# Kernel optimization log

Measured on AMD Instinct MI355X. Metric: run time of the kernel, lower is better.

The kernel has to match this reference:

```python
import jax, jax.numpy as jnp
import numpy as np

B = 16      # number of point clouds
N = 4096    # points per cloud (max after densify)
D = 3       # xyz


def setup_inputs() -> dict:
    key = jax.random.key(0)
    k1, k2 = jax.random.split(key)
    pred = jax.random.normal(k1, (B * N, D), dtype=jnp.float32)
    target = jax.random.normal(k2, (B * N, D), dtype=jnp.float32)
    # sorted segment ids, equal-sized clouds (faithful to to_dense_batch usage)
    batch = jnp.repeat(jnp.arange(B, dtype=jnp.int64), N)
    return {"pred": pred, "target": target, "batch": batch}


def to_dense_batch(x, batch, num_batches, max_n):
    # PyG to_dense_batch: scatter flat points into [B, max_n, D], zero-padded.
    ones = jnp.ones_like(batch)
    counts = jax.ops.segment_sum(ones, batch, num_segments=num_batches)
    offsets = jnp.concatenate([jnp.zeros((1,), batch.dtype), jnp.cumsum(counts)[:-1]])
    pos = jnp.arange(batch.shape[0], dtype=batch.dtype) - offsets[batch]
    dense = jnp.zeros((num_batches, max_n, x.shape[-1]), x.dtype)
    return dense.at[batch, pos].set(x)


def chamfer_distance(x, y):
    # squared-euclidean pairwise distances via the GEMM identity
    x2 = jnp.sum(x * x, axis=-1)                      # [B, N]
    y2 = jnp.sum(y * y, axis=-1)                      # [B, M]
    xy = jnp.einsum('bnd,bmd->bnm', x, y)             # [B, N, M]
    d = x2[:, :, None] + y2[:, None, :] - 2.0 * xy    # [B, N, M]
    cham_x = jnp.mean(jnp.min(d, axis=2), axis=1)     # mean over N of min over M
    cham_y = jnp.mean(jnp.min(d, axis=1), axis=1)     # mean over M of min over N
    # point_reduction='mean', batch_reduction='mean' (pytorch3d defaults)
    return jnp.mean(cham_x + cham_y)


def reference(pred, target, batch):
    x = to_dense_batch(pred, batch, B, N)
    y = to_dense_batch(target, batch, B, N)
    return chamfer_distance(x, y)
```

## Files before the change

kernel.cpp:

```cpp
#include <hip/hip_runtime.h>


namespace {

constexpr int kB = 16;
constexpr int kN = 4096;
constexpr int kPlane = kB * kN;
constexpr int kJS = 4;
constexpr int kJSL = kN / kJS;
constexpr float kScale = 1.0f / (float)(kB * kN);

typedef short bf16x8 __attribute__((ext_vector_type(8)));
typedef float f32x16 __attribute__((ext_vector_type(16)));
typedef unsigned short u16;

__device__ inline u16 bf16_rn(float f) {
  union { float f; unsigned u; } v; v.f = f;
  unsigned r = v.u + 0x7fffu + ((v.u >> 16) & 1u);
  return (u16)(r >> 16);
}
__device__ inline float bf16_f(u16 h) {
  union { unsigned u; float f; } v; v.u = (unsigned)h << 16;
  return v.f;
}
__device__ inline unsigned pk2(u16 lo, u16 hi) {
  return (unsigned)lo | ((unsigned)hi << 16);
}

__global__ void init_out(float* out) { out[0] = 0.0f; }

__global__ __launch_bounds__(256) void cd_prep(
    const float* __restrict__ pred, const float* __restrict__ targ,
    u16* __restrict__ Ab, u16* __restrict__ Bb, float* __restrict__ out) {
  const int p = blockIdx.x * 256 + threadIdx.x;
  if (p == 0) out[0] = 0.0f;
  const u16 one = 0x3F80;
  {
    const float a = pred[3 * p], c = pred[3 * p + 1], d = pred[3 * p + 2];
    const u16 ah = bf16_rn(a), ch = bf16_rn(c), dh = bf16_rn(d);
    const u16 al = bf16_rn(a - bf16_f(ah));
    const u16 cl = bf16_rn(c - bf16_f(ch));
    const u16 dl = bf16_rn(d - bf16_f(dh));
    const float s2 = fmaf(a, a, fmaf(c, c, d * d));
    const u16 s2h = bf16_rn(s2);
    const u16 s2l = bf16_rn(s2 - bf16_f(s2h));
    uint4 w0, w1;
    w0.x = pk2(ah, ch); w0.y = pk2(dh, al); w0.z = pk2(cl, dl); w0.w = pk2(ah, ch);
    w1.x = pk2(dh, s2h); w1.y = pk2(s2l, one); w1.z = pk2(one, al); w1.w = pk2(cl, dl);
    uint4* dst = reinterpret_cast<uint4*>(Ab + (size_t)p * 16);
    dst[0] = w0; dst[1] = w1;
  }
  {
    const float a = targ[3 * p], c = targ[3 * p + 1], d = targ[3 * p + 2];
    const u16 ah0 = bf16_rn(a), ch0 = bf16_rn(c), dh0 = bf16_rn(d);
    const u16 ah = bf16_rn(-2.0f * bf16_f(ah0));
    const u16 ch = bf16_rn(-2.0f * bf16_f(ch0));
    const u16 dh = bf16_rn(-2.0f * bf16_f(dh0));
    const u16 al = bf16_rn(-2.0f * bf16_f(bf16_rn(a - bf16_f(ah0))));
    const u16 cl = bf16_rn(-2.0f * bf16_f(bf16_rn(c - bf16_f(ch0))));
    const u16 dl = bf16_rn(-2.0f * bf16_f(bf16_rn(d - bf16_f(dh0))));
    const float s2 = fmaf(a, a, fmaf(c, c, d * d));
    const u16 s2h = bf16_rn(s2);
    const u16 s2l = bf16_rn(s2 - bf16_f(s2h));
    uint4 w0, w1;
    w0.x = pk2(ah, ch); w0.y = pk2(dh, ah); w0.z = pk2(ch, dh); w0.w = pk2(al, cl);
    w1.x = pk2(dl, one); w1.y = pk2(one, s2h); w1.z = pk2(s2l, al); w1.w = pk2(cl, dl);
    uint4* dst = reinterpret_cast<uint4*>(Bb + (size_t)p * 16);
    dst[0] = w0; dst[1] = w1;
  }
}

__global__ __launch_bounds__(256) void cd_mfma(
    const u16* __restrict__ Ab, const u16* __restrict__ Bb,
    float* __restrict__ colpart, float* __restrict__ rowpart) {
  __shared__ float clds[4 * kJSL];

  const int t = threadIdx.x;
  const int w = t >> 6, lane = t & 63;
  const int half = lane >> 5, l31 = lane & 31;
  const int chunk = blockIdx.x;
  const int cloud = blockIdx.y;
  const int slice = blockIdx.z;

  const int arow = cloud * kN + chunk * 128 + w * 32 + l31;
  const bf16x8 afrag = *(const bf16x8*)(Ab + (size_t)arow * 16 + half * 8);

  f32x16 zacc;
#pragma unroll
  for (int r = 0; r < 16; ++r) zacc[r] = 0.0f;
  float rmin[16];
#pragma unroll
  for (int r = 0; r < 16; ++r) rmin[r] = 1e30f;

  const u16* bbase = Bb + ((size_t)cloud * kN + slice * kJSL) * 16;
  constexpr int NT = kJSL / 64;
  const int jcol = l31 * 16 + half * 8;
  bf16x8 b0 = *(const bf16x8*)(bbase + jcol);
  bf16x8 b1 = *(const bf16x8*)(bbase + 32 * 16 + jcol);
  for (int jt = 0; jt < NT; ++jt) {
    const int nx = ((jt + 1) & (NT - 1)) * 64 * 16;
    const bf16x8 n0 = *(const bf16x8*)(bbase + nx + jcol);
    const bf16x8 n1 = *(const bf16x8*)(bbase + nx + 32 * 16 + jcol);
    const f32x16 s0 = __builtin_amdgcn_mfma_f32_32x32x16_bf16(afrag, b0, zacc, 0, 0, 0);
    const f32x16 s1 = __builtin_amdgcn_mfma_f32_32x32x16_bf16(afrag, b1, zacc, 0, 0, 0);
    float cm0 = s0[0], cm1 = s1[0];
#pragma unroll
    for (int r = 1; r < 16; ++r) { cm0 = fminf(cm0, s0[r]); cm1 = fminf(cm1, s1[r]); }
#pragma unroll
    for (int r = 0; r < 16; ++r) rmin[r] = fminf(rmin[r], fminf(s0[r], s1[r]));
    cm0 = fminf(cm0, __shfl_xor(cm0, 32, 64));
    cm1 = fminf(cm1, __shfl_xor(cm1, 32, 64));
    if (half == 0) {
      clds[w * kJSL + jt * 64 + l31] = cm0;
      clds[w * kJSL + jt * 64 + 32 + l31] = cm1;
    }
    b0 = n0; b1 = n1;
  }

#pragma unroll
  for (int st = 1; st < 32; st <<= 1) {
#pragma unroll
    for (int r = 0; r < 16; ++r)
      rmin[r] = fminf(rmin[r], __shfl_xor(rmin[r], st, 64));
  }
  if (l31 == 0) {
    float* rp = rowpart + ((size_t)slice * kB + cloud) * kN + chunk * 128 + w * 32;
#pragma unroll
    for (int r = 0; r < 16; ++r) {
      const int row = (r & 3) + 8 * (r >> 2) + 4 * half;
      rp[row] = rmin[r];
    }
  }

  __syncthreads();
  for (int j = t; j < kJSL; j += 256) {
    const float m = fminf(fminf(clds[j], clds[kJSL + j]),
                          fminf(clds[2 * kJSL + j], clds[3 * kJSL + j]));
    colpart[((size_t)cloud * 32 + chunk) * kN + slice * kJSL + j] = m;
  }
}

__global__ __launch_bounds__(256) void cd_reduce(
    const float* __restrict__ colpart, const float* __restrict__ rowpart,
    float* __restrict__ out) {
  const int u = blockIdx.x * 256 + threadIdx.x;
  const int cloud = u >> 12, p = u & (kN - 1);
  float rm = 1e30f;
#pragma unroll
  for (int s2 = 0; s2 < kJS; ++s2)
    rm = fminf(rm, rowpart[((size_t)s2 * kB + cloud) * kN + p]);
  const float* cp = colpart + (size_t)cloud * 32 * kN + p;
  float cm = 1e30f;
#pragma unroll 8
  for (int c = 0; c < 32; ++c) cm = fminf(cm, cp[(size_t)c * kN]);
  float s = rm + cm;
  for (int o = 32; o > 0; o >>= 1) s += __shfl_down(s, o, 64);
  __shared__ float wsum[4];
  const int lane = threadIdx.x & 63, wv = threadIdx.x >> 6;
  if (lane == 0) wsum[wv] = s;
  __syncthreads();
  if (threadIdx.x == 0)
    atomicAdd(out, (wsum[0] + wsum[1] + wsum[2] + wsum[3]) * kScale);
}

template <int KX>
__global__ __launch_bounds__(256) void chamfer_direct(
    const float* __restrict__ pred, const float* __restrict__ targ,
    float* __restrict__ out) {
  __shared__ float4 tA[128], tB[128];
  const int t = threadIdx.x;
  const int xb = blockIdx.x, b = blockIdx.y, dir = blockIdx.z;
  const float* __restrict__ X = dir ? targ : pred;
  const float* __restrict__ Y = dir ? pred : targ;
  float2 xx2[KX], xy2[KX], xz2[KX];
  float x2[KX], mn[KX];
  const int ibase = b * kN + xb * (256 * KX) + t;
#pragma unroll
  for (int k = 0; k < KX; ++k) {
    const int i = ibase + k * 256;
    const float a = X[3 * i], c = X[3 * i + 1], d = X[3 * i + 2];
    x2[k] = fmaf(a, a, fmaf(c, c, d * d));
    xx2[k] = make_float2(-2.0f * a, -2.0f * a);
    xy2[k] = make_float2(-2.0f * c, -2.0f * c);
    xz2[k] = make_float2(-2.0f * d, -2.0f * d);
    mn[k] = 1e30f;
  }
  for (int t0 = 0; t0 < kN; t0 += 256) {
    __syncthreads();
    if (t < 128) {
      const int j0 = 3 * (b * kN + t0 + 2 * t);
      const float a0 = Y[j0], c0 = Y[j0 + 1], d0 = Y[j0 + 2];
      const float a1 = Y[j0 + 3], c1 = Y[j0 + 4], d1 = Y[j0 + 5];
      tA[t] = make_float4(a0, a1, c0, c1);
      tB[t] = make_float4(d0, d1, fmaf(a0, a0, fmaf(c0, c0, d0 * d0)),
                          fmaf(a1, a1, fmaf(c1, c1, d1 * d1)));
    }
    __syncthreads();
    for (int jj = 0; jj < 128; ++jj) {
      const float4 qa = tA[jj], qb = tB[jj];
      const float2 qx = make_float2(qa.x, qa.y), qy = make_float2(qa.z, qa.w);
      const float2 qz = make_float2(qb.x, qb.y), qw = make_float2(qb.z, qb.w);
#pragma unroll
      for (int k = 0; k < KX; ++k) {
        float2 acc;
        asm("v_pk_fma_f32 %0, %1, %2, %3\n\t"
            "v_pk_fma_f32 %0, %4, %5, %0\n\t"
            "v_pk_fma_f32 %0, %6, %7, %0"
            : "=&v"(acc)
            : "v"(xz2[k]), "v"(qz), "v"(qw), "v"(xy2[k]), "v"(qy),
              "v"(xx2[k]), "v"(qx));
        asm("v_min3_f32 %0, %0, %1, %2" : "+v"(mn[k]) : "v"(acc.x), "v"(acc.y));
      }
    }
  }
  float s = 0.0f;
#pragma unroll
  for (int k = 0; k < KX; ++k) s += x2[k] + mn[k];
  for (int o = 32; o > 0; o >>= 1) s += __shfl_down(s, o, 64);
  __shared__ float wsum[4];
  const int lane = t & 63, wv = t >> 6;
  if (lane == 0) wsum[wv] = s;
  __syncthreads();
  if (t == 0)
    atomicAdd(out, (wsum[0] + wsum[1] + wsum[2] + wsum[3]) * kScale);
}

}

extern "C" void kernel_launch(void* const* d_in, const int* in_sizes, int n_in,
                              void* d_out, int out_size, void* d_ws,
                              size_t ws_size, hipStream_t stream) {
  const float* pred = (const float*)d_in[0];
  const float* targ = (const float*)d_in[1];
  float* out = (float*)d_out;

  const size_t needA = (size_t)kPlane * 16 * sizeof(u16);
  const size_t needCol = (size_t)kB * 32 * kN * sizeof(float);
  const size_t needRow = (size_t)kJS * kPlane * sizeof(float);
  if (ws_size >= 2 * needA + needCol + needRow) {
    u16* Ab = (u16*)d_ws;
    u16* Bb = (u16*)((char*)d_ws + needA);
    float* colpart = (float*)((char*)d_ws + 2 * needA);
    float* rowpart = (float*)((char*)d_ws + 2 * needA + needCol);
    cd_prep<<<dim3(kPlane / 256), 256, 0, stream>>>(pred, targ, Ab, Bb, out);
    cd_mfma<<<dim3(32, kB, kJS), 256, 0, stream>>>(Ab, Bb, colpart, rowpart);
    cd_reduce<<<dim3(kPlane / 256), 256, 0, stream>>>(colpart, rowpart, out);
  } else {
    init_out<<<dim3(1), dim3(1), 0, stream>>>(out);
    constexpr int KX = 8;
    dim3 grid(kN / (256 * KX), kB, 2);
    chamfer_direct<KX><<<grid, 256, 0, stream>>>(pred, targ, out);
  }
}
```

Baseline: 97.34 us.

## Fuse final reduction into MFMA kernel via atomicMin and last-block summation

Replaces the per-slice and per-chunk partial row/column min buffers with order-preserving uint-encoded atomicMin into single min arrays. The last block per cloud, found with a counter, sums the mins. This removes the separate reduce kernel launch and the large partial-buffer traffic. It also uses v_min3_f32 to cut the number of min instructions in the inner loop. In exchange it adds global atomic contention and threadfence ordering.

```diff
diff --git a/kernel.cpp b/kernel.cpp
--- a/kernel.cpp
+++ b/kernel.cpp
@@ -13,6 +13,7 @@
 typedef short bf16x8 __attribute__((ext_vector_type(8)));
 typedef float f32x16 __attribute__((ext_vector_type(16)));
 typedef unsigned short u16;
+typedef unsigned int u32;
 
 __device__ inline u16 bf16_rn(float f) {
   union { float f; unsigned u; } v; v.f = f;
@@ -27,13 +28,35 @@
   return (unsigned)lo | ((unsigned)hi << 16);
 }
 
+__device__ inline u32 fmap(float f) {
+  union { float f; u32 u; } v; v.f = f;
+  const u32 s = (u32)((int)v.u >> 31);
+  return v.u ^ (s | 0x80000000u);
+}
+__device__ inline float funmap(u32 u) {
+  union { u32 u; float f; } v;
+  v.u = (u & 0x80000000u) ? (u ^ 0x80000000u) : ~u;
+  return v.f;
+}
+
+__device__ inline float min3f(float a, float b, float c) {
+  float d;
+  asm("v_min3_f32 %0, %1, %2, %3" : "=v"(d) : "v"(a), "v"(b), "v"(c));
+  return d;
+}
+
 __global__ void init_out(float* out) { out[0] = 0.0f; }
 
 __global__ __launch_bounds__(256) void cd_prep(
     const float* __restrict__ pred, const float* __restrict__ targ,
-    u16* __restrict__ Ab, u16* __restrict__ Bb, float* __restrict__ out) {
+    u16* __restrict__ Ab, u16* __restrict__ Bb,
+    u32* __restrict__ rowmin, u32* __restrict__ colmin,
+    u32* __restrict__ cnt, float* __restrict__ out) {
   const int p = blockIdx.x * 256 + threadIdx.x;
   if (p == 0) out[0] = 0.0f;
+  if (p < kB) cnt[p] = 0u;
+  rowmin[p] = 0xFFFFFFFFu;
+  colmin[p] = 0xFFFFFFFFu;
   const u16 one = 0x3F80;
   {
     const float a = pred[3 * p], c = pred[3 * p + 1], d = pred[3 * p + 2];
@@ -72,8 +95,11 @@
 
 __global__ __launch_bounds__(256) void cd_mfma(
     const u16* __restrict__ Ab, const u16* __restrict__ Bb,
-    float* __restrict__ colpart, float* __restrict__ rowpart) {
+    u32* __restrict__ rowmin, u32* __restrict__ colmin,
+    u32* __restrict__ cnt, float* __restrict__ out) {
   __shared__ float clds[4 * kJSL];
+  __shared__ int lastflag;
+  __shared__ float wsum[4];
 
   const int t = threadIdx.x;
   const int w = t >> 6, lane = t & 63;
@@ -103,11 +129,21 @@
     const bf16x8 n1 = *(const bf16x8*)(bbase + nx + 32 * 16 + jcol);
     const f32x16 s0 = __builtin_amdgcn_mfma_f32_32x32x16_bf16(afrag, b0, zacc, 0, 0, 0);
     const f32x16 s1 = __builtin_amdgcn_mfma_f32_32x32x16_bf16(afrag, b1, zacc, 0, 0, 0);
-    float cm0 = s0[0], cm1 = s1[0];
-#pragma unroll
-    for (int r = 1; r < 16; ++r) { cm0 = fminf(cm0, s0[r]); cm1 = fminf(cm1, s1[r]); }
-#pragma unroll
-    for (int r = 0; r < 16; ++r) rmin[r] = fminf(rmin[r], fminf(s0[r], s1[r]));
+    float a0 = min3f(s0[0], s0[1], s0[2]);
+    float a1 = min3f(s0[3], s0[4], s0[5]);
+    float a2 = min3f(s0[6], s0[7], s0[8]);
+    float a3 = min3f(s0[9], s0[10], s0[11]);
+    float a4 = min3f(s0[12], s0[13], s0[14]);
+    float cm0 = fminf(min3f(a0, a1, a2), min3f(a3, a4, s0[15]));
+    float b0t = min3f(s1[0], s1[1], s1[2]);
+    float b1t = min3f(s1[3], s1[4], s1[5]);
+    float b2t = min3f(s1[6], s1[7], s1[8]);
+    float b3t = min3f(s1[9], s1[10], s1[11]);
+    float b4t = min3f(s1[12], s1[13], s1[14]);
+    float cm1 = fminf(min3f(b0t, b1t, b2t), min3f(b3t, b4t, s1[15]));
+#pragma unroll
+    for (int r = 0; r < 16; ++r)
+      asm("v_min3_f32 %0, %0, %1, %2" : "+v"(rmin[r]) : "v"(s0[r]), "v"(s1[r]));
     cm0 = fminf(cm0, __shfl_xor(cm0, 32, 64));
     cm1 = fminf(cm1, __shfl_xor(cm1, 32, 64));
     if (half == 0) {
@@ -124,11 +160,11 @@
       rmin[r] = fminf(rmin[r], __shfl_xor(rmin[r], st, 64));
   }
   if (l31 == 0) {
-    float* rp = rowpart + ((size_t)slice * kB + cloud) * kN + chunk * 128 + w * 32;
+    u32* rp = rowmin + (size_t)cloud * kN + chunk * 128 + w * 32;
 #pragma unroll
     for (int r = 0; r < 16; ++r) {
       const int row = (r & 3) + 8 * (r >> 2) + 4 * half;
-      rp[row] = rmin[r];
+      atomicMin(&rp[row], fmap(rmin[r]));
     }
   }
 
@@ -136,31 +172,33 @@
   for (int j = t; j < kJSL; j += 256) {
     const float m = fminf(fminf(clds[j], clds[kJSL + j]),
                           fminf(clds[2 * kJSL + j], clds[3 * kJSL + j]));
-    colpart[((size_t)cloud * 32 + chunk) * kN + slice * kJSL + j] = m;
-  }
-}
-
-__global__ __launch_bounds__(256) void cd_reduce(
-    const float* __restrict__ colpart, const float* __restrict__ rowpart,
-    float* __restrict__ out) {
-  const int u = blockIdx.x * 256 + threadIdx.x;
-  const int cloud = u >> 12, p = u & (kN - 1);
-  float rm = 1e30f;
-#pragma unroll
-  for (int s2 = 0; s2 < kJS; ++s2)
-    rm = fminf(rm, rowpart[((size_t)s2 * kB + cloud) * kN + p]);
-  const float* cp = colpart + (size_t)cloud * 32 * kN + p;
-  float cm = 1e30f;
-#pragma unroll 8
-  for (int c = 0; c < 32; ++c) cm = fminf(cm, cp[(size_t)c * kN]);
-  float s = rm + cm;
-  for (int o = 32; o > 0; o >>= 1) s += __shfl_down(s, o, 64);
-  __shared__ float wsum[4];
-  const int lane = threadIdx.x & 63, wv = threadIdx.x >> 6;
-  if (lane == 0) wsum[wv] = s;
-  __syncthreads();
-  if (threadIdx.x == 0)
-    atomicAdd(out, (wsum[0] + wsum[1] + wsum[2] + wsum[3]) * kScale);
+    atomicMin(&colmin[(size_t)cloud * kN + slice * kJSL + j], fmap(m));
+  }
+
+  __syncthreads();
+  if (t == 0) {
+    __threadfence();
+    lastflag = (atomicAdd(&cnt[cloud], 1u) == (u32)(32 * kJS - 1)) ? 1 : 0;
+  }
+  __syncthreads();
+  if (lastflag) {
+    __threadfence();
+    u32* rm = rowmin + (size_t)cloud * kN;
+    u32* cm = colmin + (size_t)cloud * kN;
+    float s = 0.0f;
+    for (int p = t; p < kN; p += 256) {
+      const u32 a = __hip_atomic_load(&rm[p], __ATOMIC_RELAXED,
+                                      __HIP_MEMORY_SCOPE_AGENT);
+      const u32 b = __hip_atomic_load(&cm[p], __ATOMIC_RELAXED,
+                                      __HIP_MEMORY_SCOPE_AGENT);
+      s += funmap(a) + funmap(b);
+    }
+    for (int o = 32; o > 0; o >>= 1) s += __shfl_down(s, o, 64);
+    if (lane == 0) wsum[w] = s;
+    __syncthreads();
+    if (t == 0)
+      atomicAdd(out, (wsum[0] + wsum[1] + wsum[2] + wsum[3]) * kScale);
+  }
 }
 
 template <int KX>
@@ -235,16 +273,18 @@
   float* out = (float*)d_out;
 
   const size_t needA = (size_t)kPlane * 16 * sizeof(u16);
-  const size_t needCol = (size_t)kB * 32 * kN * sizeof(float);
-  const size_t needRow = (size_t)kJS * kPlane * sizeof(float);
-  if (ws_size >= 2 * needA + needCol + needRow) {
+  const size_t needMin = (size_t)kPlane * sizeof(u32);
+  const size_t needCnt = 256;
+  if (ws_size >= 2 * needA + 2 * needMin + needCnt) {
     u16* Ab = (u16*)d_ws;
     u16* Bb = (u16*)((char*)d_ws + needA);
-    float* colpart = (float*)((char*)d_ws + 2 * needA);
-    float* rowpart = (float*)((char*)d_ws + 2 * needA + needCol);
-    cd_prep<<<dim3(kPlane / 256), 256, 0, stream>>>(pred, targ, Ab, Bb, out);
-    cd_mfma<<<dim3(32, kB, kJS), 256, 0, stream>>>(Ab, Bb, colpart, rowpart);
-    cd_reduce<<<dim3(kPlane / 256), 256, 0, stream>>>(colpart, rowpart, out);
+    u32* rowmin = (u32*)((char*)d_ws + 2 * needA);
+    u32* colmin = (u32*)((char*)d_ws + 2 * needA + needMin);
+    u32* cnt = (u32*)((char*)d_ws + 2 * needA + 2 * needMin);
+    cd_prep<<<dim3(kPlane / 256), 256, 0, stream>>>(pred, targ, Ab, Bb,
+                                                    rowmin, colmin, cnt, out);
+    cd_mfma<<<dim3(32, kB, kJS), 256, 0, stream>>>(Ab, Bb, rowmin, colmin,
+                                                   cnt, out);
   } else {
     init_out<<<dim3(1), dim3(1), 0, stream>>>(out);
     constexpr int KX = 8;
```

After: 137.5 us. 1.41x slower.

## Compute both chamfer directions as row-min with LDS-staged B tiles

Applied to the files above, without the earlier changes.

Replaces the column-min partial buffers and separate reduce kernel by running the MFMA kernel twice (pred→targ and targ→pred), each only doing row minima and atomically summing. B operands are pre-laid-out per 512-point stage and double-buffered into LDS via global_load_lds, and row minima use v_min3. This doubles MFMA work but removes column reductions, the colpart/rowpart traffic and one launch; the grid drops from 4 slices to 2 directions, so each block loops over all 4096 columns.

```diff
diff --git a/kernel.cpp b/kernel.cpp
--- a/kernel.cpp
+++ b/kernel.cpp
@@ -6,8 +6,8 @@
 constexpr int kB = 16;
 constexpr int kN = 4096;
 constexpr int kPlane = kB * kN;
-constexpr int kJS = 4;
-constexpr int kJSL = kN / kJS;
+constexpr int kStage = 512;
+constexpr int kNS = kN / kStage;
 constexpr float kScale = 1.0f / (float)(kB * kN);
 
 typedef short bf16x8 __attribute__((ext_vector_type(8)));
@@ -31,12 +31,23 @@
 
 __global__ __launch_bounds__(256) void cd_prep(
     const float* __restrict__ pred, const float* __restrict__ targ,
-    u16* __restrict__ Ab, u16* __restrict__ Bb, float* __restrict__ out) {
+    u16* __restrict__ Apred, u16* __restrict__ Atarg,
+    u16* __restrict__ Bpred, u16* __restrict__ Btarg,
+    float* __restrict__ out) {
   const int p = blockIdx.x * 256 + threadIdx.x;
   if (p == 0) out[0] = 0.0f;
+  const int cloud = p >> 12, q = p & (kN - 1);
+  const int stg = q >> 9, pl = q & (kStage - 1);
+  const size_t boff = (size_t)cloud * 65536 + (size_t)stg * 8192 + (size_t)pl * 8;
   const u16 one = 0x3F80;
-  {
-    const float a = pred[3 * p], c = pred[3 * p + 1], d = pred[3 * p + 2];
+
+  const float* srcs[2] = {pred, targ};
+  u16* adsts[2] = {Apred, Atarg};
+  u16* bdsts[2] = {Bpred, Btarg};
+#pragma unroll
+  for (int which = 0; which < 2; ++which) {
+    const float a = srcs[which][3 * p], c = srcs[which][3 * p + 1],
+                d = srcs[which][3 * p + 2];
     const u16 ah = bf16_rn(a), ch = bf16_rn(c), dh = bf16_rn(d);
     const u16 al = bf16_rn(a - bf16_f(ah));
     const u16 cl = bf16_rn(c - bf16_f(ch));
@@ -44,46 +55,65 @@
     const float s2 = fmaf(a, a, fmaf(c, c, d * d));
     const u16 s2h = bf16_rn(s2);
     const u16 s2l = bf16_rn(s2 - bf16_f(s2h));
-    uint4 w0, w1;
-    w0.x = pk2(ah, ch); w0.y = pk2(dh, al); w0.z = pk2(cl, dl); w0.w = pk2(ah, ch);
-    w1.x = pk2(dh, s2h); w1.y = pk2(s2l, one); w1.z = pk2(one, al); w1.w = pk2(cl, dl);
-    uint4* dst = reinterpret_cast<uint4*>(Ab + (size_t)p * 16);
-    dst[0] = w0; dst[1] = w1;
-  }
-  {
-    const float a = targ[3 * p], c = targ[3 * p + 1], d = targ[3 * p + 2];
-    const u16 ah0 = bf16_rn(a), ch0 = bf16_rn(c), dh0 = bf16_rn(d);
-    const u16 ah = bf16_rn(-2.0f * bf16_f(ah0));
-    const u16 ch = bf16_rn(-2.0f * bf16_f(ch0));
-    const u16 dh = bf16_rn(-2.0f * bf16_f(dh0));
-    const u16 al = bf16_rn(-2.0f * bf16_f(bf16_rn(a - bf16_f(ah0))));
-    const u16 cl = bf16_rn(-2.0f * bf16_f(bf16_rn(c - bf16_f(ch0))));
-    const u16 dl = bf16_rn(-2.0f * bf16_f(bf16_rn(d - bf16_f(dh0))));
-    const float s2 = fmaf(a, a, fmaf(c, c, d * d));
-    const u16 s2h = bf16_rn(s2);
-    const u16 s2l = bf16_rn(s2 - bf16_f(s2h));
-    uint4 w0, w1;
-    w0.x = pk2(ah, ch); w0.y = pk2(dh, ah); w0.z = pk2(ch, dh); w0.w = pk2(al, cl);
-    w1.x = pk2(dl, one); w1.y = pk2(one, s2h); w1.z = pk2(s2l, al); w1.w = pk2(cl, dl);
-    uint4* dst = reinterpret_cast<uint4*>(Bb + (size_t)p * 16);
-    dst[0] = w0; dst[1] = w1;
+    {
+      uint4 w0, w1;
+      w0.x = pk2(ah, ch); w0.y = pk2(dh, al); w0.z = pk2(cl, dl); w0.w = pk2(ah, ch);
+      w1.x = pk2(dh, s2h); w1.y = pk2(s2l, one); w1.z = pk2(one, al); w1.w = pk2(cl, dl);
+      uint4* dst = reinterpret_cast<uint4*>(adsts[which] + (size_t)p * 16);
+      dst[0] = w0; dst[1] = w1;
+    }
+    {
+      const u16 nah = bf16_rn(-2.0f * bf16_f(ah));
+      const u16 nch = bf16_rn(-2.0f * bf16_f(ch));
+      const u16 ndh = bf16_rn(-2.0f * bf16_f(dh));
+      const u16 nal = bf16_rn(-2.0f * bf16_f(al));
+      const u16 ncl = bf16_rn(-2.0f * bf16_f(cl));
+      const u16 ndl = bf16_rn(-2.0f * bf16_f(dl));
+      uint4 w0, w1;
+      w0.x = pk2(nah, nch); w0.y = pk2(ndh, nah); w0.z = pk2(nch, ndh); w0.w = pk2(nal, ncl);
+      w1.x = pk2(ndl, one); w1.y = pk2(one, s2h); w1.z = pk2(s2l, nal); w1.w = pk2(ncl, ndl);
+      *reinterpret_cast<uint4*>(bdsts[which] + boff) = w0;
+      *reinterpret_cast<uint4*>(bdsts[which] + boff + 4096) = w1;
+    }
   }
 }
 
 __global__ __launch_bounds__(256) void cd_mfma(
-    const u16* __restrict__ Ab, const u16* __restrict__ Bb,
-    float* __restrict__ colpart, float* __restrict__ rowpart) {
-  __shared__ float clds[4 * kJSL];
+    const u16* __restrict__ Apred, const u16* __restrict__ Atarg,
+    const u16* __restrict__ Bpred, const u16* __restrict__ Btarg,
+    float* __restrict__ out) {
+  __shared__ uint4 Blds4[2048];
+  __shared__ float wsum[4];
 
   const int t = threadIdx.x;
   const int w = t >> 6, lane = t & 63;
   const int half = lane >> 5, l31 = lane & 31;
   const int chunk = blockIdx.x;
   const int cloud = blockIdx.y;
-  const int slice = blockIdx.z;
+  const int dir = blockIdx.z;
+  const u16* __restrict__ A = dir ? Atarg : Apred;
+  const u16* __restrict__ B = dir ? Bpred : Btarg;
 
   const int arow = cloud * kN + chunk * 128 + w * 32 + l31;
-  const bf16x8 afrag = *(const bf16x8*)(Ab + (size_t)arow * 16 + half * 8);
+  union { uint4 u; bf16x8 v; } afu;
+  afu.u = *reinterpret_cast<const uint4*>(A + (size_t)arow * 16 + half * 8);
+  const bf16x8 afrag = afu.v;
+
+  const char* bcloud = (const char*)B + (size_t)cloud * 131072;
+  char* ldsbase = (char*)Blds4;
+#define STAGE(st, buf)                                                        \
+  {                                                                           \
+    const char* _src = bcloud + (size_t)(st) * 16384;                         \
+    char* _dst = ldsbase + (buf) * 16384;                                     \
+    _Pragma("unroll")                                                         \
+    for (int i = 0; i < 4; ++i) {                                             \
+      __builtin_amdgcn_global_load_lds(                                       \
+          (const __attribute__((address_space(1))) void*)(_src +              \
+              ((w * 4 + i) * 64 + lane) * 16),                                \
+          (__attribute__((address_space(3))) void*)(_dst + (w * 4 + i) * 1024),\
+          16, 0, 0);                                                          \
+    }                                                                         \
+  }
 
   f32x16 zacc;
 #pragma unroll
@@ -92,30 +122,29 @@
 #pragma unroll
   for (int r = 0; r < 16; ++r) rmin[r] = 1e30f;
 
-  const u16* bbase = Bb + ((size_t)cloud * kN + slice * kJSL) * 16;
-  constexpr int NT = kJSL / 64;
-  const int jcol = l31 * 16 + half * 8;
-  bf16x8 b0 = *(const bf16x8*)(bbase + jcol);
-  bf16x8 b1 = *(const bf16x8*)(bbase + 32 * 16 + jcol);
-  for (int jt = 0; jt < NT; ++jt) {
-    const int nx = ((jt + 1) & (NT - 1)) * 64 * 16;
-    const bf16x8 n0 = *(const bf16x8*)(bbase + nx + jcol);
-    const bf16x8 n1 = *(const bf16x8*)(bbase + nx + 32 * 16 + jcol);
-    const f32x16 s0 = __builtin_amdgcn_mfma_f32_32x32x16_bf16(afrag, b0, zacc, 0, 0, 0);
-    const f32x16 s1 = __builtin_amdgcn_mfma_f32_32x32x16_bf16(afrag, b1, zacc, 0, 0, 0);
-    float cm0 = s0[0], cm1 = s1[0];
-#pragma unroll
-    for (int r = 1; r < 16; ++r) { cm0 = fminf(cm0, s0[r]); cm1 = fminf(cm1, s1[r]); }
-#pragma unroll
-    for (int r = 0; r < 16; ++r) rmin[r] = fminf(rmin[r], fminf(s0[r], s1[r]));
-    cm0 = fminf(cm0, __shfl_xor(cm0, 32, 64));
-    cm1 = fminf(cm1, __shfl_xor(cm1, 32, 64));
-    if (half == 0) {
-      clds[w * kJSL + jt * 64 + l31] = cm0;
-      clds[w * kJSL + jt * 64 + 32 + l31] = cm1;
-    }
-    b0 = n0; b1 = n1;
-  }
+  STAGE(0, 0);
+  __syncthreads();
+
+  for (int st = 0; st < kNS; ++st) {
+    if (st < kNS - 1) STAGE(st + 1, (st + 1) & 1);
+    const char* blc = ldsbase + (st & 1) * 16384 + half * 8192 + l31 * 16;
+#pragma unroll
+    for (int jt = 0; jt < kStage / 64; ++jt) {
+      union { uint4 u; bf16x8 v; } B0, B1;
+      B0.u = *reinterpret_cast<const uint4*>(blc + jt * 1024);
+      B1.u = *reinterpret_cast<const uint4*>(blc + jt * 1024 + 512);
+      const f32x16 s0 =
+          __builtin_amdgcn_mfma_f32_32x32x16_bf16(afrag, B0.v, zacc, 0, 0, 0);
+      const f32x16 s1 =
+          __builtin_amdgcn_mfma_f32_32x32x16_bf16(afrag, B1.v, zacc, 0, 0, 0);
+#pragma unroll
+      for (int r = 0; r < 16; ++r)
+        asm("v_min3_f32 %0, %0, %1, %2"
+            : "+v"(rmin[r]) : "v"(s0[r]), "v"(s1[r]));
+    }
+    __syncthreads();
+  }
+#undef STAGE
 
 #pragma unroll
   for (int st = 1; st < 32; st <<= 1) {
@@ -123,43 +152,14 @@
     for (int r = 0; r < 16; ++r)
       rmin[r] = fminf(rmin[r], __shfl_xor(rmin[r], st, 64));
   }
-  if (l31 == 0) {
-    float* rp = rowpart + ((size_t)slice * kB + cloud) * kN + chunk * 128 + w * 32;
-#pragma unroll
-    for (int r = 0; r < 16; ++r) {
-      const int row = (r & 3) + 8 * (r >> 2) + 4 * half;
-      rp[row] = rmin[r];
-    }
-  }
-
+  float s = 0.0f;
+#pragma unroll
+  for (int r = 0; r < 16; ++r) s += rmin[r];
+  s = (l31 == 0) ? s : 0.0f;
+  s += __shfl_down(s, 32, 64);
+  if (lane == 0) wsum[w] = s;
   __syncthreads();
-  for (int j = t; j < kJSL; j += 256) {
-    const float m = fminf(fminf(clds[j], clds[kJSL + j]),
-                          fminf(clds[2 * kJSL + j], clds[3 * kJSL + j]));
-    colpart[((size_t)cloud * 32 + chunk) * kN + slice * kJSL + j] = m;
-  }
-}
-
-__global__ __launch_bounds__(256) void cd_reduce(
-    const float* __restrict__ colpart, const float* __restrict__ rowpart,
-    float* __restrict__ out) {
-  const int u = blockIdx.x * 256 + threadIdx.x;
-  const int cloud = u >> 12, p = u & (kN - 1);
-  float rm = 1e30f;
-#pragma unroll
-  for (int s2 = 0; s2 < kJS; ++s2)
-    rm = fminf(rm, rowpart[((size_t)s2 * kB + cloud) * kN + p]);
-  const float* cp = colpart + (size_t)cloud * 32 * kN + p;
-  float cm = 1e30f;
-#pragma unroll 8
-  for (int c = 0; c < 32; ++c) cm = fminf(cm, cp[(size_t)c * kN]);
-  float s = rm + cm;
-  for (int o = 32; o > 0; o >>= 1) s += __shfl_down(s, o, 64);
-  __shared__ float wsum[4];
-  const int lane = threadIdx.x & 63, wv = threadIdx.x >> 6;
-  if (lane == 0) wsum[wv] = s;
-  __syncthreads();
-  if (threadIdx.x == 0)
+  if (t == 0)
     atomicAdd(out, (wsum[0] + wsum[1] + wsum[2] + wsum[3]) * kScale);
 }
 
@@ -234,17 +234,16 @@
   const float* targ = (const float*)d_in[1];
   float* out = (float*)d_out;
 
-  const size_t needA = (size_t)kPlane * 16 * sizeof(u16);
-  const size_t needCol = (size_t)kB * 32 * kN * sizeof(float);
-  const size_t needRow = (size_t)kJS * kPlane * sizeof(float);
-  if (ws_size >= 2 * needA + needCol + needRow) {
-    u16* Ab = (u16*)d_ws;
-    u16* Bb = (u16*)((char*)d_ws + needA);
-    float* colpart = (float*)((char*)d_ws + 2 * needA);
-    float* rowpart = (float*)((char*)d_ws + 2 * needA + needCol);
-    cd_prep<<<dim3(kPlane / 256), 256, 0, stream>>>(pred, targ, Ab, Bb, out);
-    cd_mfma<<<dim3(32, kB, kJS), 256, 0, stream>>>(Ab, Bb, colpart, rowpart);
-    cd_reduce<<<dim3(kPlane / 256), 256, 0, stream>>>(colpart, rowpart, out);
+  const size_t needOne = (size_t)kPlane * 16 * sizeof(u16);
+  if (ws_size >= 4 * needOne) {
+    u16* Apred = (u16*)d_ws;
+    u16* Atarg = (u16*)((char*)d_ws + needOne);
+    u16* Bpred = (u16*)((char*)d_ws + 2 * needOne);
+    u16* Btarg = (u16*)((char*)d_ws + 3 * needOne);
+    cd_prep<<<dim3(kPlane / 256), 256, 0, stream>>>(pred, targ, Apred, Atarg,
+                                                    Bpred, Btarg, out);
+    cd_mfma<<<dim3(32, kB, 2), 256, 0, stream>>>(Apred, Atarg, Bpred, Btarg,
+                                                 out);
   } else {
     init_out<<<dim3(1), dim3(1), 0, stream>>>(out);
     constexpr int KX = 8;
```

New measurement: 94.92 us. 1.03x faster.
